# Optimization experiments

Measured on AMD Instinct MI355X. Metric: run time of the kernel, lower is better.

The kernel has to match this reference:

```python
import jax, jax.numpy as jnp
import numpy as np

D_MODEL = 1024
NUM_HEADS = 16
HEAD_DIM = D_MODEL // NUM_HEADS


def setup_inputs() -> dict:
    key = jax.random.key(0)
    ks = jax.random.split(key, 9)
    B, S = 2, 2048
    s = 1.0 / np.sqrt(D_MODEL)
    return {
        "x": jax.random.normal(ks[0], (B, S, D_MODEL), dtype=jnp.float32),
        "Wq": jax.random.normal(ks[1], (D_MODEL, D_MODEL), dtype=jnp.float32) * s,
        "bq": jnp.zeros((D_MODEL,), dtype=jnp.float32),
        "Wk": jax.random.normal(ks[2], (D_MODEL, D_MODEL), dtype=jnp.float32) * s,
        "bk": jnp.zeros((D_MODEL,), dtype=jnp.float32),
        "Wv": jax.random.normal(ks[3], (D_MODEL, D_MODEL), dtype=jnp.float32) * s,
        "bv": jnp.zeros((D_MODEL,), dtype=jnp.float32),
        "Wo": jax.random.normal(ks[4], (D_MODEL, D_MODEL), dtype=jnp.float32) * s,
        "bo": jnp.zeros((D_MODEL,), dtype=jnp.float32),
    }


def reference(x, Wq, bq, Wk, bk, Wv, bv, Wo, bo):
    B, S, _ = x.shape
    # linear projections then split heads: [B, S, D] -> [B, H, S, hd]
    def split_heads(t):
        return t.reshape(B, S, NUM_HEADS, HEAD_DIM).transpose(0, 2, 1, 3)
    q = split_heads(x @ Wq + bq)
    k = split_heads(x @ Wk + bk)
    v = split_heads(x @ Wv + bv)
    # scores: [B, H, S, S]
    scores = jnp.einsum('bhqd,bhkd->bhqk', q, k) / jnp.sqrt(
        jnp.asarray(HEAD_DIM, dtype=x.dtype))
    attn = jax.nn.softmax(scores, axis=-1)
    # dropout is identity in eval mode
    out = jnp.einsum('bhqk,bhkd->bhqd', attn, v)
    out = out.transpose(0, 2, 1, 3).reshape(B, S, D_MODEL)
    return out @ Wo + bo
```

## Files before the change

### kernel.cpp

```cpp
#include <hip/hip_runtime.h>

#define D_MODEL 1024
#define NHEAD 16
#define HD 64
#define BATCH 2
#define SEQ 2048

typedef unsigned short u16;
typedef unsigned int u32;
typedef __bf16 bf16x8 __attribute__((ext_vector_type(8)));
typedef unsigned short u16x8 __attribute__((ext_vector_type(8)));
typedef short s16x4 __attribute__((ext_vector_type(4)));
typedef float f32x4 __attribute__((ext_vector_type(4)));

#if defined(__has_builtin)
#if __has_builtin(__builtin_amdgcn_exp2f)
#define EXP2(x) __builtin_amdgcn_exp2f(x)
#else
#define EXP2(x) exp2f(x)
#endif
#else
#define EXP2(x) exp2f(x)
#endif

static __device__ __forceinline__ u16 f2bf(float f) {
    union { float f; unsigned u; } v; v.f = f;
    unsigned u = v.u;
    u += 0x7fffu + ((u >> 16) & 1u);
    return (u16)(u >> 16);
}

static __device__ __forceinline__ void gld_lds16(const void* g, void* l) {
    __builtin_amdgcn_global_load_lds(
        (const __attribute__((address_space(1))) void*)g,
        (__attribute__((address_space(3))) void*)l, 16, 0, 0);
}

static __device__ __forceinline__ bf16x8 pack_bf8(f32x4 a, f32x4 b) {
    union { float f; unsigned u; } a0, a1, a2, a3, b0, b1, b2, b3;
    a0.f = a[0]; a1.f = a[1]; a2.f = a[2]; a3.f = a[3];
    b0.f = b[0]; b1.f = b[1]; b2.f = b[2]; b3.f = b[3];
    union { unsigned u[4]; bf16x8 v; } r;
    r.u[0] = __builtin_amdgcn_perm(a1.u, a0.u, 0x07060302u);
    r.u[1] = __builtin_amdgcn_perm(a3.u, a2.u, 0x07060302u);
    r.u[2] = __builtin_amdgcn_perm(b1.u, b0.u, 0x07060302u);
    r.u[3] = __builtin_amdgcn_perm(b3.u, b2.u, 0x07060302u);
    return r.v;
}

__global__ __launch_bounds__(256) void k_convert(const float* __restrict__ x,
                                                 const float* __restrict__ wq,
                                                 const float* __restrict__ wk,
                                                 const float* __restrict__ wv,
                                                 const float* __restrict__ wo,
                                                 u16* __restrict__ xb,
                                                 u16* __restrict__ wt) {
    int z = blockIdx.z;
    if (z == 0) {
        int base = (blockIdx.y * 32 + blockIdx.x) * 256 + threadIdx.x;
#pragma unroll
        for (int p = 0; p < 4; p++) {
            int i = base + p * 262144;
            float4 v = ((const float4*)x)[i];
            ushort4 o = make_ushort4(f2bf(v.x), f2bf(v.y), f2bf(v.z), f2bf(v.w));
            ((ushort4*)xb)[i] = o;
        }
        return;
    }
    __shared__ u16 t[32][33];
    const float* W = z == 1 ? wq : z == 2 ? wk : z == 3 ? wv : wo;
    u16* dst = wt + (size_t)(z - 1) * (D_MODEL * D_MODEL);
    int tx = threadIdx.x & 31, ty = threadIdx.x >> 5;
    int n0 = blockIdx.x * 32, k0 = blockIdx.y * 32;
#pragma unroll
    for (int i = 0; i < 4; i++)
        t[ty + i * 8][tx] = f2bf(W[(size_t)(k0 + ty + i * 8) * D_MODEL + n0 + tx]);
    __syncthreads();
#pragma unroll
    for (int i = 0; i < 4; i++)
        dst[(size_t)(n0 + ty + i * 8) * D_MODEL + k0 + tx] = t[tx][ty + i * 8];
}

__global__ __launch_bounds__(256) void k_gemm(const u16* __restrict__ A,
                                              const u16* __restrict__ WtBase,
                                              const float* __restrict__ b0,
                                              const float* __restrict__ b1,
                                              const float* __restrict__ b2,
                                              u16* __restrict__ oq, u16* __restrict__ ok,
                                              u16* __restrict__ ov) {
    __shared__ u16 lA[2 * 128 * 32];
    __shared__ u16 lB[2 * 128 * 32];
    int tid = threadIdx.x, w = tid >> 6, l = tid & 63, lr = l & 15, lq = l >> 4;
    int z = blockIdx.z;
    const u16* Wt = WtBase + (size_t)z * (D_MODEL * D_MODEL);
    const float* bias = z == 0 ? b0 : z == 1 ? b1 : b2;
    float scale = (z == 0) ? (0.125f * 1.44269504088896340736f) : 1.0f;
    int m0 = blockIdx.y * 128, n0 = blockIdx.x * 128;
    int wm = (w >> 1) * 64, wn = (w & 1) * 64;
    f32x4 acc[4][4];
#pragma unroll
    for (int mi = 0; mi < 4; mi++)
#pragma unroll
        for (int ni = 0; ni < 4; ni++) acc[mi][ni] = (f32x4){0.f, 0.f, 0.f, 0.f};

    int ra = tid >> 2, ca = (tid & 3) * 8;
    for (int kk = 0; kk < D_MODEL; kk += 64) {
#pragma unroll
        for (int kc = 0; kc < 2; kc++) {
            int cg = kk + kc * 32 + ca;
            gld_lds16(A + (size_t)(m0 + ra) * D_MODEL + cg, &lA[kc * 4096 + w * 512]);
            gld_lds16(A + (size_t)(m0 + 64 + ra) * D_MODEL + cg,
                      &lA[kc * 4096 + 2048 + w * 512]);
            gld_lds16(Wt + (size_t)(n0 + ra) * D_MODEL + cg, &lB[kc * 4096 + w * 512]);
            gld_lds16(Wt + (size_t)(n0 + 64 + ra) * D_MODEL + cg,
                      &lB[kc * 4096 + 2048 + w * 512]);
        }
        __syncthreads();
#pragma unroll
        for (int kc = 0; kc < 2; kc++) {
            bf16x8 af[4], bf[4];
#pragma unroll
            for (int mi = 0; mi < 4; mi++)
                af[mi] = *(const bf16x8*)&lA[kc * 4096 + (wm + mi * 16 + lr) * 32 + lq * 8];
#pragma unroll
            for (int ni = 0; ni < 4; ni++)
                bf[ni] = *(const bf16x8*)&lB[kc * 4096 + (wn + ni * 16 + lr) * 32 + lq * 8];
#pragma unroll
            for (int mi = 0; mi < 4; mi++)
#pragma unroll
                for (int ni = 0; ni < 4; ni++)
                    acc[mi][ni] = __builtin_amdgcn_mfma_f32_16x16x32_bf16(
                        af[mi], bf[ni], acc[mi][ni], 0, 0, 0);
        }
        __syncthreads();
    }
#pragma unroll
    for (int mi = 0; mi < 4; mi++) {
#pragma unroll
        for (int ni = 0; ni < 4; ni++) {
            int col = n0 + wn + ni * 16 + lr;
            float bval = bias[col];
            int row0 = m0 + wm + mi * 16 + lq * 4;
            if (z == 2) {
                int b = row0 >> 11, s = row0 & 2047;
                int h = col >> 6, dd = col & 63;
                ushort4 pk;
                pk.x = f2bf(acc[mi][ni][0] + bval);
                pk.y = f2bf(acc[mi][ni][1] + bval);
                pk.z = f2bf(acc[mi][ni][2] + bval);
                pk.w = f2bf(acc[mi][ni][3] + bval);
                *(ushort4*)&ov[((size_t)(b * NHEAD + h) * HD + dd) * SEQ + s] = pk;
            } else {
#pragma unroll
                for (int r = 0; r < 4; r++) {
                    int row = row0 + r;
                    float val = (acc[mi][ni][r] + bval) * scale;
                    u16* op = z == 0 ? oq : ok;
                    int b = row >> 11, s = row & 2047, h = col >> 6, d = col & 63;
                    op[(((size_t)(b * NHEAD + h)) * SEQ + s) * HD + d] = f2bf(val);
                }
            }
        }
    }
}

__global__ __launch_bounds__(256) void k_gout(const u16* __restrict__ A,
                                              const u16* __restrict__ Wt,
                                              const float* __restrict__ bias,
                                              float* __restrict__ outf) {
    __shared__ u16 lA[64 * 32];
    __shared__ u16 lB[64 * 32];
    int tid = threadIdx.x, w = tid >> 6, l = tid & 63, lr = l & 15, lq = l >> 4;
    int m0 = blockIdx.y * 64, n0 = blockIdx.x * 64;
    int wm = (w >> 1) * 32, wn = (w & 1) * 32;
    f32x4 acc[2][2];
#pragma unroll
    for (int mi = 0; mi < 2; mi++)
#pragma unroll
        for (int ni = 0; ni < 2; ni++) acc[mi][ni] = (f32x4){0.f, 0.f, 0.f, 0.f};

    int ra = tid >> 2, ca = (tid & 3) * 8;
    for (int kk = 0; kk < D_MODEL; kk += 32) {
        gld_lds16(A + (size_t)(m0 + ra) * D_MODEL + kk + ca, &lA[w * 512]);
        gld_lds16(Wt + (size_t)(n0 + ra) * D_MODEL + kk + ca, &lB[w * 512]);
        __syncthreads();
        bf16x8 af[2], bf[2];
#pragma unroll
        for (int mi = 0; mi < 2; mi++)
            af[mi] = *(const bf16x8*)&lA[(wm + mi * 16 + lr) * 32 + lq * 8];
#pragma unroll
        for (int ni = 0; ni < 2; ni++)
            bf[ni] = *(const bf16x8*)&lB[(wn + ni * 16 + lr) * 32 + lq * 8];
#pragma unroll
        for (int mi = 0; mi < 2; mi++)
#pragma unroll
            for (int ni = 0; ni < 2; ni++)
                acc[mi][ni] = __builtin_amdgcn_mfma_f32_16x16x32_bf16(
                    af[mi], bf[ni], acc[mi][ni], 0, 0, 0);
        __syncthreads();
    }
#pragma unroll
    for (int mi = 0; mi < 2; mi++)
#pragma unroll
        for (int ni = 0; ni < 2; ni++) {
            int col = n0 + wn + ni * 16 + lr;
            float bval = bias[col];
#pragma unroll
            for (int r = 0; r < 4; r++) {
                int row = m0 + wm + mi * 16 + lq * 4 + r;
                outf[(size_t)row * D_MODEL + col] = acc[mi][ni][r] + bval;
            }
        }
}

static __device__ __forceinline__ int ksw(int row, int col) {
    return row * 64 + ((((col >> 3) ^ (row & 7)) << 3) | (col & 7));
}
static __device__ __forceinline__ int vsw(int row, int col) {
    return row * 128 + ((((col >> 3) ^ (row & 15)) << 3) | (col & 7));
}

__global__ __launch_bounds__(256) void k_attn(const u16* __restrict__ Q,
                                              const u16* __restrict__ K,
                                              const u16* __restrict__ VT,
                                              u16* __restrict__ part0,
                                              u16* __restrict__ part1,
                                              float* __restrict__ lsum, int nsplit) {
    __shared__ __align__(16) u16 lK[128 * 64];
    __shared__ __align__(16) u16 lVt[64 * 128];
    int tid = threadIdx.x, w = tid >> 6, l = tid & 63, lr = l & 15, lq = l >> 4;
    int bl = blockIdx.x;
    int qt = bl / (32 * nsplit);
    int rem = bl - qt * (32 * nsplit);
    int bh = rem / nsplit;
    int ks = rem - bh * nsplit;
    int qb = qt * 128 + w * 32;
    const u16* Qb = Q + (size_t)bh * SEQ * HD;
    const u16* Kb = K + (size_t)bh * SEQ * HD;
    const u16* VTb = VT + (size_t)bh * HD * SEQ;

    bf16x8 qf[2][2];
#pragma unroll
    for (int tq = 0; tq < 2; tq++)
#pragma unroll
        for (int kc = 0; kc < 2; kc++)
            qf[tq][kc] = *(const bf16x8*)&Qb[(size_t)(qb + tq * 16 + lr) * HD +
                                             kc * 32 + lq * 8];
    f32x4 o[2][4];
    f32x4 ol[2];
#pragma unroll
    for (int tq = 0; tq < 2; tq++) {
        ol[tq] = (f32x4){0.f, 0.f, 0.f, 0.f};
#pragma unroll
        for (int di = 0; di < 4; di++) o[tq][di] = (f32x4){0.f, 0.f, 0.f, 0.f};
    }
    union { u16 s[8]; bf16x8 v; } onev;
#pragma unroll
    for (int i = 0; i < 8; i++) onev.s[i] = 0x3F80;
    const bf16x8 vone8 = onev.v;

    int krow = tid >> 3, kch = tid & 7;
    int vrow = tid >> 4, vch = tid & 15;

    int nk = SEQ / nsplit;
    int jbeg = ks * nk, jend = jbeg + nk;

    u16x8 kreg[4], vreg[4];
#pragma unroll
    for (int p = 0; p < 4; p++) {
        kreg[p] = *(const u16x8*)&Kb[(size_t)(jbeg + p * 32 + krow) * HD + kch * 8];
        vreg[p] = *(const u16x8*)&VTb[(size_t)(p * 16 + vrow) * SEQ + jbeg + vch * 8];
    }

    for (int j0 = jbeg; j0 < jend; j0 += 128) {
        __syncthreads();
#pragma unroll
        for (int p = 0; p < 4; p++) {
            *(u16x8*)&lK[ksw(p * 32 + krow, kch * 8)] = kreg[p];
            *(u16x8*)&lVt[vsw(p * 16 + vrow, vch * 8)] = vreg[p];
        }
        __syncthreads();
        if (j0 + 128 < jend) {
            int jn = j0 + 128;
#pragma unroll
            for (int p = 0; p < 4; p++) {
                kreg[p] = *(const u16x8*)&Kb[(size_t)(jn + p * 32 + krow) * HD + kch * 8];
                vreg[p] = *(const u16x8*)&VTb[(size_t)(p * 16 + vrow) * SEQ + jn + vch * 8];
            }
        }

#pragma unroll
        for (int kh = 0; kh < 2; kh++) {
#pragma unroll
            for (int t2 = 0; t2 < 2; t2++) {
                int rA = kh * 64 + t2 * 32 + lr;
                int rB = rA + 16;
                bf16x8 kA0 = *(const bf16x8*)&lK[ksw(rA, lq * 8)];
                bf16x8 kA1 = *(const bf16x8*)&lK[ksw(rA, 32 + lq * 8)];
                bf16x8 kB0 = *(const bf16x8*)&lK[ksw(rB, lq * 8)];
                bf16x8 kB1 = *(const bf16x8*)&lK[ksw(rB, 32 + lq * 8)];
                f32x4 sA0 = (f32x4){0.f, 0.f, 0.f, 0.f};
                f32x4 sA1 = (f32x4){0.f, 0.f, 0.f, 0.f};
                f32x4 sB0 = (f32x4){0.f, 0.f, 0.f, 0.f};
                f32x4 sB1 = (f32x4){0.f, 0.f, 0.f, 0.f};
                __builtin_amdgcn_s_setprio(1);
                sA0 = __builtin_amdgcn_mfma_f32_16x16x32_bf16(kA0, qf[0][0], sA0, 0, 0, 0);
                sB0 = __builtin_amdgcn_mfma_f32_16x16x32_bf16(kB0, qf[0][0], sB0, 0, 0, 0);
                sA1 = __builtin_amdgcn_mfma_f32_16x16x32_bf16(kA0, qf[1][0], sA1, 0, 0, 0);
                sB1 = __builtin_amdgcn_mfma_f32_16x16x32_bf16(kB0, qf[1][0], sB1, 0, 0, 0);
                sA0 = __builtin_amdgcn_mfma_f32_16x16x32_bf16(kA1, qf[0][1], sA0, 0, 0, 0);
                sB0 = __builtin_amdgcn_mfma_f32_16x16x32_bf16(kB1, qf[0][1], sB0, 0, 0, 0);
                sA1 = __builtin_amdgcn_mfma_f32_16x16x32_bf16(kA1, qf[1][1], sA1, 0, 0, 0);
                sB1 = __builtin_amdgcn_mfma_f32_16x16x32_bf16(kB1, qf[1][1], sB1, 0, 0, 0);
                __builtin_amdgcn_s_setprio(0);
#pragma unroll
                for (int r = 0; r < 4; r++) {
                    sA0[r] = EXP2(sA0[r]);
                    sA1[r] = EXP2(sA1[r]);
                    sB0[r] = EXP2(sB0[r]);
                    sB1[r] = EXP2(sB1[r]);
                }
                bf16x8 pf0 = pack_bf8(sA0, sB0);
                bf16x8 pf1 = pack_bf8(sA1, sB1);
                __builtin_amdgcn_s_setprio(1);
                ol[0] = __builtin_amdgcn_mfma_f32_16x16x32_bf16(pf0, vone8, ol[0], 0, 0, 0);
                ol[1] = __builtin_amdgcn_mfma_f32_16x16x32_bf16(pf1, vone8, ol[1], 0, 0, 0);
#pragma unroll
                for (int di = 0; di < 4; di++) {
                    int vr = di * 16 + lr;
                    union { bf16x8 v; s16x4 h[2]; } vv;
                    vv.h[0] = *(const s16x4*)&lVt[vsw(vr, kh * 64 + t2 * 32 + lq * 4)];
                    vv.h[1] = *(const s16x4*)&lVt[vsw(vr, kh * 64 + t2 * 32 + 16 + lq * 4)];
                    o[0][di] = __builtin_amdgcn_mfma_f32_16x16x32_bf16(pf0, vv.v,
                                                                       o[0][di], 0, 0, 0);
                    o[1][di] = __builtin_amdgcn_mfma_f32_16x16x32_bf16(pf1, vv.v,
                                                                       o[1][di], 0, 0, 0);
                }
                __builtin_amdgcn_s_setprio(0);
            }
        }
    }
    int b = bh >> 4, h = bh & 15;
    if (nsplit == 1) {
#pragma unroll
        for (int tq = 0; tq < 2; tq++) {
#pragma unroll
            for (int di = 0; di < 4; di++)
#pragma unroll
                for (int r = 0; r < 4; r++) {
                    int qg = qb + tq * 16 + lq * 4 + r;
                    part0[((size_t)(b * SEQ + qg)) * D_MODEL + h * 64 + di * 16 + lr] =
                        f2bf(o[tq][di][r] / ol[tq][r]);
                }
        }
    } else {
        u16* pdst = (ks == 0) ? part0 : part1;
#pragma unroll
        for (int tq = 0; tq < 2; tq++)
#pragma unroll
            for (int di = 0; di < 4; di++)
#pragma unroll
                for (int r = 0; r < 4; r++) {
                    int qg = qb + tq * 16 + lq * 4 + r;
                    union { _Float16 h; u16 u; } cv;
                    cv.h = (_Float16)o[tq][di][r];
                    pdst[((size_t)(b * SEQ + qg)) * D_MODEL + h * 64 + di * 16 + lr] =
                        cv.u;
                }
        if (lr == 0) {
#pragma unroll
            for (int tq = 0; tq < 2; tq++)
#pragma unroll
                for (int r = 0; r < 4; r++) {
                    int qg = qb + tq * 16 + lq * 4 + r;
                    lsum[(ks * 32 + bh) * 2048 + qg] = ol[tq][r];
                }
        }
    }
}

__global__ __launch_bounds__(256) void k_combine(const u16* __restrict__ p0,
                                                 const u16* __restrict__ p1,
                                                 const float* __restrict__ lsum,
                                                 u16* __restrict__ dst) {
    int i = blockIdx.x * 256 + threadIdx.x;
    size_t a8 = (size_t)i * 8;
    int row = (int)(a8 >> 10);
    int col = (int)(a8 & 1023);
    int b = row >> 11, q = row & 2047, h = col >> 6;
    int mi = ((b << 4) + h) * 2048 + q;
    float inv = 1.0f / (lsum[mi] + lsum[65536 + mi]);
    u16x8 h0 = *(const u16x8*)(p0 + a8);
    u16x8 h1 = *(const u16x8*)(p1 + a8);
    u16x8 out;
#pragma unroll
    for (int j = 0; j < 8; j++) {
        union { _Float16 h; u16 u; } c0, c1;
        c0.u = h0[j]; c1.u = h1[j];
        out[j] = f2bf(((float)c0.h + (float)c1.h) * inv);
    }
    *(u16x8*)(dst + a8) = out;
}

extern "C" void kernel_launch(void* const* d_in, const int* in_sizes, int n_in,
                              void* d_out, int out_size, void* d_ws, size_t ws_size,
                              hipStream_t stream) {
    const float* x  = (const float*)d_in[0];
    const float* Wq = (const float*)d_in[1];
    const float* bq = (const float*)d_in[2];
    const float* Wk = (const float*)d_in[3];
    const float* bk = (const float*)d_in[4];
    const float* Wv = (const float*)d_in[5];
    const float* bv = (const float*)d_in[6];
    const float* Wo = (const float*)d_in[7];
    const float* bo = (const float*)d_in[8];
    float* out = (float*)d_out;

    char* ws = (char*)d_ws;
    u16* xb  = (u16*)ws;
    u16* wt  = (u16*)(ws + (size_t)8 * 1024 * 1024);
    u16* qws = (u16*)(ws + (size_t)16 * 1024 * 1024);
    u16* kws = (u16*)(ws + (size_t)24 * 1024 * 1024);
    u16* vtw = (u16*)(ws + (size_t)32 * 1024 * 1024);
    u16* ao  = (u16*)(ws + (size_t)40 * 1024 * 1024);
    float* ml = (float*)(ws + (size_t)48 * 1024 * 1024);

    int nsplit = (ws_size >= (size_t)49 * 1024 * 1024) ? 2 : 1;
    u16* attn_out = (nsplit == 2) ? xb : ao;

    k_convert<<<dim3(32, 32, 5), 256, 0, stream>>>(x, Wq, Wk, Wv, Wo, xb, wt);
    k_gemm<<<dim3(8, 32, 3), 256, 0, stream>>>(xb, wt, bq, bk, bv, qws, kws, vtw);
    if (nsplit == 2) {
        k_attn<<<16 * 32 * 2, 256, 0, stream>>>(qws, kws, vtw, xb, ao, ml, 2);
        k_combine<<<2048, 256, 0, stream>>>(xb, ao, ml, xb);
    } else {
        k_attn<<<16 * 32, 256, 0, stream>>>(qws, kws, vtw, ao, nullptr, ml, 1);
    }
    k_gout<<<dim3(16, 64), 256, 0, stream>>>(attn_out,
                                             wt + (size_t)3 * D_MODEL * D_MODEL,
                                             bo, out);
}
```

Before: 205.7 us.

## Double-buffer LDS tiles in QKV and output projection GEMMs

Both projection GEMM kernels now stage the next K-slice into a second LDS buffer while MFMAs run on the current one. This hides global-to-LDS load latency behind compute and needs one barrier per step. The QKV kernel moves from 64-wide K steps with two sub-chunks to 32-wide steps with a ping-pong buffer. s_setprio is also raised around the MFMA block. The risk is that gld_lds16 completion may not be properly waited on before the barrier, and the output GEMM's LDS use doubles.

New measurement: 190.6 us. 1.08x faster.

```diff
diff --git a/kernel.cpp b/kernel.cpp
--- a/kernel.cpp
+++ b/kernel.cpp
@@ -104,35 +104,40 @@
         for (int ni = 0; ni < 4; ni++) acc[mi][ni] = (f32x4){0.f, 0.f, 0.f, 0.f};
 
     int ra = tid >> 2, ca = (tid & 3) * 8;
-    for (int kk = 0; kk < D_MODEL; kk += 64) {
-#pragma unroll
-        for (int kc = 0; kc < 2; kc++) {
-            int cg = kk + kc * 32 + ca;
-            gld_lds16(A + (size_t)(m0 + ra) * D_MODEL + cg, &lA[kc * 4096 + w * 512]);
-            gld_lds16(A + (size_t)(m0 + 64 + ra) * D_MODEL + cg,
-                      &lA[kc * 4096 + 2048 + w * 512]);
-            gld_lds16(Wt + (size_t)(n0 + ra) * D_MODEL + cg, &lB[kc * 4096 + w * 512]);
-            gld_lds16(Wt + (size_t)(n0 + 64 + ra) * D_MODEL + cg,
-                      &lB[kc * 4096 + 2048 + w * 512]);
-        }
+    const u16* Aba = A + (size_t)(m0 + ra) * D_MODEL + ca;
+    const u16* Abb = A + (size_t)(m0 + 64 + ra) * D_MODEL + ca;
+    const u16* Bba = Wt + (size_t)(n0 + ra) * D_MODEL + ca;
+    const u16* Bbb = Wt + (size_t)(n0 + 64 + ra) * D_MODEL + ca;
+
+    auto stage = [&](int kk, int buf) {
+        gld_lds16(Aba + kk, &lA[buf * 4096 + w * 512]);
+        gld_lds16(Abb + kk, &lA[buf * 4096 + 2048 + w * 512]);
+        gld_lds16(Bba + kk, &lB[buf * 4096 + w * 512]);
+        gld_lds16(Bbb + kk, &lB[buf * 4096 + 2048 + w * 512]);
+    };
+
+    stage(0, 0);
+    __syncthreads();
+    int cur = 0;
+    for (int t = 0; t < 32; ++t) {
+        if (t + 1 < 32) stage((t + 1) * 32, cur ^ 1);
+        bf16x8 af[4], bf[4];
+#pragma unroll
+        for (int mi = 0; mi < 4; mi++)
+            af[mi] = *(const bf16x8*)&lA[cur * 4096 + (wm + mi * 16 + lr) * 32 + lq * 8];
+#pragma unroll
+        for (int ni = 0; ni < 4; ni++)
+            bf[ni] = *(const bf16x8*)&lB[cur * 4096 + (wn + ni * 16 + lr) * 32 + lq * 8];
+        __builtin_amdgcn_s_setprio(1);
+#pragma unroll
+        for (int mi = 0; mi < 4; mi++)
+#pragma unroll
+            for (int ni = 0; ni < 4; ni++)
+                acc[mi][ni] = __builtin_amdgcn_mfma_f32_16x16x32_bf16(
+                    af[mi], bf[ni], acc[mi][ni], 0, 0, 0);
+        __builtin_amdgcn_s_setprio(0);
         __syncthreads();
-#pragma unroll
-        for (int kc = 0; kc < 2; kc++) {
-            bf16x8 af[4], bf[4];
-#pragma unroll
-            for (int mi = 0; mi < 4; mi++)
-                af[mi] = *(const bf16x8*)&lA[kc * 4096 + (wm + mi * 16 + lr) * 32 + lq * 8];
-#pragma unroll
-            for (int ni = 0; ni < 4; ni++)
-                bf[ni] = *(const bf16x8*)&lB[kc * 4096 + (wn + ni * 16 + lr) * 32 + lq * 8];
-#pragma unroll
-            for (int mi = 0; mi < 4; mi++)
-#pragma unroll
-                for (int ni = 0; ni < 4; ni++)
-                    acc[mi][ni] = __builtin_amdgcn_mfma_f32_16x16x32_bf16(
-                        af[mi], bf[ni], acc[mi][ni], 0, 0, 0);
-        }
-        __syncthreads();
+        cur ^= 1;
     }
 #pragma unroll
     for (int mi = 0; mi < 4; mi++) {
@@ -168,8 +173,8 @@
                                               const u16* __restrict__ Wt,
                                               const float* __restrict__ bias,
                                               float* __restrict__ outf) {
-    __shared__ u16 lA[64 * 32];
-    __shared__ u16 lB[64 * 32];
+    __shared__ u16 lA[2 * 64 * 32];
+    __shared__ u16 lB[2 * 64 * 32];
     int tid = threadIdx.x, w = tid >> 6, l = tid & 63, lr = l & 15, lq = l >> 4;
     int m0 = blockIdx.y * 64, n0 = blockIdx.x * 64;
     int wm = (w >> 1) * 32, wn = (w & 1) * 32;
@@ -180,24 +185,36 @@
         for (int ni = 0; ni < 2; ni++) acc[mi][ni] = (f32x4){0.f, 0.f, 0.f, 0.f};
 
     int ra = tid >> 2, ca = (tid & 3) * 8;
-    for (int kk = 0; kk < D_MODEL; kk += 32) {
-        gld_lds16(A + (size_t)(m0 + ra) * D_MODEL + kk + ca, &lA[w * 512]);
-        gld_lds16(Wt + (size_t)(n0 + ra) * D_MODEL + kk + ca, &lB[w * 512]);
-        __syncthreads();
+    const u16* Aba = A + (size_t)(m0 + ra) * D_MODEL + ca;
+    const u16* Bba = Wt + (size_t)(n0 + ra) * D_MODEL + ca;
+
+    auto stage = [&](int kk, int buf) {
+        gld_lds16(Aba + kk, &lA[buf * 2048 + w * 512]);
+        gld_lds16(Bba + kk, &lB[buf * 2048 + w * 512]);
+    };
+
+    stage(0, 0);
+    __syncthreads();
+    int cur = 0;
+    for (int t = 0; t < 32; ++t) {
+        if (t + 1 < 32) stage((t + 1) * 32, cur ^ 1);
         bf16x8 af[2], bf[2];
 #pragma unroll
         for (int mi = 0; mi < 2; mi++)
-            af[mi] = *(const bf16x8*)&lA[(wm + mi * 16 + lr) * 32 + lq * 8];
+            af[mi] = *(const bf16x8*)&lA[cur * 2048 + (wm + mi * 16 + lr) * 32 + lq * 8];
 #pragma unroll
         for (int ni = 0; ni < 2; ni++)
-            bf[ni] = *(const bf16x8*)&lB[(wn + ni * 16 + lr) * 32 + lq * 8];
+            bf[ni] = *(const bf16x8*)&lB[cur * 2048 + (wn + ni * 16 + lr) * 32 + lq * 8];
+        __builtin_amdgcn_s_setprio(1);
 #pragma unroll
         for (int mi = 0; mi < 2; mi++)
 #pragma unroll
             for (int ni = 0; ni < 2; ni++)
                 acc[mi][ni] = __builtin_amdgcn_mfma_f32_16x16x32_bf16(
                     af[mi], bf[ni], acc[mi][ni], 0, 0, 0);
+        __builtin_amdgcn_s_setprio(0);
         __syncthreads();
+        cur ^= 1;
     }
 #pragma unroll
     for (int mi = 0; mi < 2; mi++)
```
